# Performance work log

Hardware: AMD Instinct MI355X
Metric: run time of the kernel (lower is better)

Reference implementation:

```python
import jax, jax.numpy as jnp
import numpy as np

# Detect() defaults from the source
NUM_CLASSES = 2
TOP_K = 750          # max detections returned per class
NMS_TOP_K = 5000     # candidates considered by NMS
NMS_THRESH = 0.3
CONF_THRESH = 0.05
VAR0, VAR1 = 0.1, 0.2  # prior box variances


def decode(loc, priors):
    # loc, priors: [P,4]; priors in (cx,cy,w,h); returns corner boxes [P,4]
    xy = priors[:, :2] + loc[:, :2] * VAR0 * priors[:, 2:]
    wh = priors[:, 2:] * jnp.exp(loc[:, 2:] * VAR1)
    x1y1 = xy - wh * 0.5
    x2y2 = x1y1 + wh
    return jnp.concatenate([x1y1, x2y2], axis=1)


def nms_single(boxes, scores):
    # boxes [P,4], scores [P] -> kept rows [TOP_K,5] = (score, x1,y1,x2,y2)
    s = jnp.where(scores > CONF_THRESH, scores, -1.0)
    top_s, top_i = jax.lax.top_k(s, NMS_TOP_K)   # restrict to best nms_top_k candidates
    cb = boxes[top_i]                             # [K,4] candidate boxes
    area = (cb[:, 2] - cb[:, 0]) * (cb[:, 3] - cb[:, 1])
    ar = jnp.arange(NMS_TOP_K)

    def step(s_cur, _):
        i = jnp.argmax(s_cur)                     # highest-scoring unsuppressed box
        sc = s_cur[i]
        ok = sc > 0.0                             # any valid candidate left?
        b = cb[i]
        xx1 = jnp.maximum(cb[:, 0], b[0])
        yy1 = jnp.maximum(cb[:, 1], b[1])
        xx2 = jnp.minimum(cb[:, 2], b[2])
        yy2 = jnp.minimum(cb[:, 3], b[3])
        inter = jnp.clip(xx2 - xx1, 0.0) * jnp.clip(yy2 - yy1, 0.0)
        union = area - inter + area[i]
        iou = inter / union
        supp = (iou > NMS_THRESH) | (ar == i)     # suppress overlapping + self
        s_next = jnp.where(ok & supp, -1.0, s_cur)
        row = jnp.where(ok, jnp.concatenate([sc[None], b]), jnp.zeros(5, boxes.dtype))
        return s_next, row

    _, rows = jax.lax.scan(step, top_s, None, length=TOP_K)
    return rows  # [TOP_K, 5]


def setup_inputs() -> dict:
    key = jax.random.key(0)
    k1, k2, k3 = jax.random.split(key, 3)
    B, P = 8, 136500
    loc_data = jax.random.normal(k1, (B, P, 4), jnp.float32)
    conf_data = jax.random.normal(k2, (B, P, 2), jnp.float32)
    u = jax.random.uniform(k3, (P, 4), jnp.float32)
    # priors: cx,cy in (0,1); w,h small positive (normalized coords)
    prior_data = jnp.concatenate([u[:, :2], u[:, 2:] * 0.1 + 0.01], axis=1)
    return {"loc_data": loc_data, "conf_data": conf_data, "prior_data": prior_data}


def reference(loc_data, conf_data, prior_data):
    B = loc_data.shape[0]
    conf = jax.nn.softmax(conf_data, axis=-1)                    # [B,P,2]
    boxes = jax.vmap(lambda l: decode(l, prior_data))(loc_data)  # [B,P,4]
    rows = jax.vmap(nms_single)(boxes, conf[:, :, 1])            # [B,TOP_K,5]
    out = jnp.zeros((B, NUM_CLASSES, TOP_K, 5), loc_data.dtype)  # class 0 = background, all zeros
    out = out.at[:, 1].set(rows)
    return out
```

## Files before the change

kernel.cpp:

```cpp
#include <hip/hip_runtime.h>
#include <stdint.h>

#pragma clang fp contract(off)

#define NPRI   136500
#define BATCH  8
#define NMS_K  5000
#define NKPAD  5120
#define TOPK   750
#define SORT_N 8192
#define HBINS  1024
#define HOFF   0x3D40
#define MROW   80
#define CNTSTRIDE 32
#define CUT    32

typedef unsigned long long u64;

__device__ __forceinline__ u64 shfl64(u64 v, int src) {
    int lo = __shfl((int)(unsigned)(v & 0xffffffffull), src);
    int hi = __shfl((int)(unsigned)(v >> 32), src);
    return ((u64)(unsigned)hi << 32) | (u64)(unsigned)lo;
}
__device__ __forceinline__ u64 shfl64_xor(u64 v, int m) {
    int lo = __shfl_xor((int)(unsigned)(v & 0xffffffffull), m);
    int hi = __shfl_xor((int)(unsigned)(v >> 32), m);
    return ((u64)(unsigned)hi << 32) | (u64)(unsigned)lo;
}

__device__ __forceinline__ bool iou_sup(float4 c4, float aj,
                                        float4 rbx, float ra) {
    float xx1 = fmaxf(c4.x, rbx.x);
    float yy1 = fmaxf(c4.y, rbx.y);
    float xx2 = fminf(c4.z, rbx.z);
    float yy2 = fminf(c4.w, rbx.w);
    float iw = fmaxf(xx2 - xx1, 0.0f);
    float ih = fmaxf(yy2 - yy1, 0.0f);
    float inter = iw * ih;
    float uni = (aj - inter) + ra;
    float u = fmaf(-0.3f, uni, inter);
    float d = fmaf(-1.4901161193847656e-8f, uni, u);
    return d > 0.0f;
}
__device__ __forceinline__ u64 iou_word(float4 c4, float aj,
                                        float4 rbx, float ra) {
    return __ballot(iou_sup(c4, aj, rbx, ra));
}

__device__ __forceinline__ u64 diag_mask(u64 word, int sh) {
    if (sh >= 0)
        word &= (sh >= 63) ? 0ull : (~0ull << (sh + 1));
    return word;
}

__device__ u64 row_word_slow(const float4* __restrict__ cbp,
                             const float* __restrict__ cap,
                             float4 rbx, float ra, int W) {
    int jbase = W << 6;
    u64 word = 0ull;
    for (int jj = 0; jj < 64; ++jj) {
        int jc = min(jbase + jj, NMS_K - 1);
        if (iou_sup(cbp[jc], cap[jc], rbx, ra)) word |= (1ull << jj);
    }
    return word;
}

__global__ __launch_bounds__(256) void score_hist_kernel(
        const float* __restrict__ conf, unsigned int* __restrict__ hist,
        float* __restrict__ sraw) {
    int b = blockIdx.y;
    __shared__ unsigned int h[HBINS];
    for (int i = threadIdx.x; i < HBINS; i += 256) h[i] = 0;
    __syncthreads();
    for (int p = blockIdx.x * 256 + threadIdx.x; p < NPRI; p += 64 * 256) {
        float2 c = ((const float2*)conf)[(size_t)b * NPRI + p];
        float m  = fmaxf(c.x, c.y);
        float e0 = expf(c.x - m), e1 = expf(c.y - m);
        float s  = e1 / (e0 + e1);
        sraw[(size_t)b * NPRI + p] = s;
        if (s > 0.05f) {
            int bin = (int)(__float_as_uint(s) >> 16) - HOFF;
            bin = min(max(bin, 0), HBINS - 1);
            atomicAdd(&h[bin], 1u);
        }
    }
    __syncthreads();
    for (int i = threadIdx.x; i < HBINS; i += 256) {
        unsigned int v = h[i];
        if (v) atomicAdd(&hist[b * HBINS + i], v);
    }
}

__global__ __launch_bounds__(256) void compact_kernel(
        const float* __restrict__ sraw, const unsigned int* __restrict__ hist,
        u64* __restrict__ keys, unsigned int* __restrict__ cnt) {
    int b = blockIdx.y;
    int tid = threadIdx.x;
    int lane = tid & 63;
    __shared__ u64 buf[2304];
    __shared__ unsigned int hsum[256];
    __shared__ int best_sh;
    __shared__ unsigned int nloc;
    __shared__ unsigned int base_sh;
    const unsigned int* hb = hist + b * HBINS;
    int t4 = tid * 4;
    unsigned int h0 = hb[t4], h1 = hb[t4 + 1], h2 = hb[t4 + 2], h3 = hb[t4 + 3];
    hsum[tid] = h0 + h1 + h2 + h3;
    if (tid == 0) { best_sh = 0; nloc = 0; }
    __syncthreads();
    for (int o = 1; o < 256; o <<= 1) {
        unsigned int add = (tid + o < 256) ? hsum[tid + o] : 0u;
        __syncthreads();
        hsum[tid] += add;
        __syncthreads();
    }
    unsigned int nxt = (tid + 1 < 256) ? hsum[tid + 1] : 0u;
    unsigned int s3 = h3 + nxt;
    unsigned int s2 = h2 + s3;
    unsigned int s1 = h1 + s2;
    unsigned int s0 = h0 + s1;
    int cand = -1;
    if (s3 >= (unsigned)NMS_K) cand = t4 + 3;
    else if (s2 >= (unsigned)NMS_K) cand = t4 + 2;
    else if (s1 >= (unsigned)NMS_K) cand = t4 + 1;
    else if (s0 >= (unsigned)NMS_K) cand = t4;
    if (cand > 0) atomicMax(&best_sh, cand);
    __syncthreads();
    int tb = best_sh;
    for (int p = blockIdx.x * 256 + tid; p < NPRI; p += 64 * 256) {
        float s = sraw[(size_t)b * NPRI + p];
        bool pass = false;
        unsigned int bits = 0;
        if (s > 0.05f) {
            bits = __float_as_uint(s);
            int bin = (int)(bits >> 16) - HOFF;
            bin = min(max(bin, 0), HBINS - 1);
            pass = (bin >= tb);
        }
        u64 bal = __ballot(pass);
        int rank = (int)__popcll(bal & ((1ull << lane) - 1ull));
        unsigned int wbase = 0;
        if (lane == 0 && bal)
            wbase = atomicAdd(&nloc, (unsigned)__popcll(bal));
        wbase = (unsigned)__shfl((int)wbase, 0);
        if (pass)
            buf[wbase + rank] = ((u64)bits << 32) | (u64)(~(unsigned int)p);
    }
    __syncthreads();
    unsigned int tot = nloc;
    if (tid == 0)
        base_sh = tot ? atomicAdd(&cnt[b * CNTSTRIDE], tot) : 0u;
    __syncthreads();
    unsigned int base = base_sh;
    for (unsigned int i = tid; i < tot; i += 256) {
        unsigned int pos = base + i;
        if (pos < SORT_N)
            keys[(size_t)b * SORT_N + pos] = buf[i];
    }
}

__global__ __launch_bounds__(512) void sortmerge2k_kernel(
        const u64* __restrict__ keys, u64* __restrict__ keys2,
        const unsigned int* __restrict__ cnt) {
    int b = blockIdx.y, c = blockIdx.x;
    int tid = threadIdx.x;
    int lane = tid & 63;
    int wv = tid >> 6;
    int n = min((int)cnt[b * CNTSTRIDE], SORT_N);
    int base = c * 2048;
    if (base >= n) {
        for (int i = tid; i < 2048; i += 512)
            keys2[(size_t)b * SORT_N + base + i] = 0ull;
        return;
    }
    __shared__ u64 k[2048];
    __shared__ u64 k2[2048];
    for (int ch = wv; ch < 32; ch += 8) {
        int idx = base + ch * 64 + lane;
        u64 v = (idx < n) ? keys[(size_t)b * SORT_N + idx] : 0ull;
#pragma unroll
        for (int kk = 2; kk <= 64; kk <<= 1) {
#pragma unroll
            for (int j = kk >> 1; j > 0; j >>= 1) {
                u64 o = shfl64_xor(v, j);
                bool low  = (lane & j) == 0;
                bool desc = (lane & kk) == 0;
                u64 mx = (v >= o) ? v : o;
                u64 mn = (v >= o) ? o : v;
                v = desc ? (low ? mx : mn) : (low ? mn : mx);
            }
        }
        k[ch * 64 + lane] = v;
    }
    __syncthreads();
    u64* src = k;
    u64* dst = k2;
    for (int L = 64; L < 2048; L <<= 1) {
        for (int o = tid; o < 2048; o += 512) {
            int pair = o / (2 * L);
            int oo = o - pair * 2 * L;
            const u64* A  = src + pair * 2 * L;
            const u64* Bp = A + L;
            int lo = max(0, oo - L), hi = min(oo, L);
            while (lo < hi) {
                int mid = (lo + hi + 1) >> 1;
                bool ok = (oo - mid >= L) || (A[mid - 1] >= Bp[oo - mid]);
                if (ok) lo = mid; else hi = mid - 1;
            }
            int i = lo, j = oo - lo;
            u64 v;
            if (j >= L) v = A[i];
            else if (i >= L) v = Bp[j];
            else v = (A[i] >= Bp[j]) ? A[i] : Bp[j];
            dst[o] = v;
        }
        __syncthreads();
        u64* t = src; src = dst; dst = t;
    }
    for (int i = tid; i < 2048; i += 512)
        keys2[(size_t)b * SORT_N + base + i] = src[i];
}

__global__ __launch_bounds__(256) void merge1_kernel(
        const u64* __restrict__ keys2, u64* __restrict__ keys) {
    int b = blockIdx.y;
    int o = blockIdx.x * 256 + threadIdx.x;
    int pair = o >> 12;
    int oo = o & 4095;
    const u64* A  = keys2 + (size_t)b * SORT_N + pair * 4096;
    const u64* Bp = A + 2048;
    int lo = max(0, oo - 2048), hi = min(oo, 2048);
    while (lo < hi) {
        int mid = (lo + hi + 1) >> 1;
        bool ok = (oo - mid >= 2048) || (A[mid - 1] >= Bp[oo - mid]);
        if (ok) lo = mid; else hi = mid - 1;
    }
    int i = lo, j = oo - lo;
    u64 v;
    if (j >= 2048) v = A[i];
    else if (i >= 2048) v = Bp[j];
    else v = (A[i] >= Bp[j]) ? A[i] : Bp[j];
    keys[(size_t)b * SORT_N + pair * 4096 + oo] = v;
}

__global__ __launch_bounds__(256) void merge2_decode_kernel(
        const u64* __restrict__ keys,
        const float* __restrict__ loc, const float* __restrict__ priors,
        float* __restrict__ cscore, float* __restrict__ cbox,
        float* __restrict__ carea) {
    int b = blockIdx.y;
    int o = blockIdx.x * 256 + threadIdx.x;
    const u64* A  = keys + (size_t)b * SORT_N;
    const u64* Bp = A + 4096;
    int lo = max(0, o - 4096), hi = min(o, 4096);
    while (lo < hi) {
        int mid = (lo + hi + 1) >> 1;
        bool ok = (o - mid >= 4096) || (A[mid - 1] >= Bp[o - mid]);
        if (ok) lo = mid; else hi = mid - 1;
    }
    int i = lo, j = o - lo;
    u64 key;
    if (j >= 4096) key = A[i];
    else if (i >= 4096) key = Bp[j];
    else key = (A[i] >= Bp[j]) ? A[i] : Bp[j];
    if (o >= NMS_K) return;
    float sc; int idx;
    if (key != 0ull) {
        sc  = __uint_as_float((unsigned int)(key >> 32));
        idx = (int)(~(unsigned int)key);
    } else { sc = -1.0f; idx = 0; }
    cscore[b * NMS_K + o] = sc;
    float x1 = 0.f, y1 = 0.f, x2 = 0.f, y2 = 0.f, ar = 0.f;
    if (key != 0ull) {
        const float* l  = loc + ((size_t)b * NPRI + idx) * 4;
        const float* pr = priors + (size_t)idx * 4;
        float lx = l[0], ly = l[1], lw = l[2], lh = l[3];
        float pcx = pr[0], pcy = pr[1], pw = pr[2], ph = pr[3];
        float cx = pcx + (lx * 0.1f) * pw;
        float cy = pcy + (ly * 0.1f) * ph;
        float wd = pw * expf(lw * 0.2f);
        float ht = ph * expf(lh * 0.2f);
        x1 = cx - wd * 0.5f;  y1 = cy - ht * 0.5f;
        x2 = x1 + wd;         y2 = y1 + ht;
        ar = (x2 - x1) * (y2 - y1);
    }
    float* cb = cbox + ((size_t)b * NMS_K + o) * 4;
    cb[0] = x1; cb[1] = y1; cb[2] = x2; cb[3] = y2;
    carea[b * NMS_K + o] = ar;
}

__global__ __launch_bounds__(256, 4) void maskbuild_kernel(
        const float* __restrict__ cbox, const float* __restrict__ carea,
        u64* __restrict__ M) {
    int b   = blockIdx.y;
    int bid = blockIdx.x;
    int wgq, rb;
    if (bid >= 380) { wgq = 19; rb = bid - 380; }
    else {
        int w = (int)((sqrtf((float)(4 * bid + 5)) - 1.0f) * 0.5f);
        while (w * (w + 1) > bid) w--;
        while ((w + 1) * (w + 2) <= bid) w++;
        wgq = w; rb = bid - w * (w + 1);
    }
    int tid  = threadIdx.x;
    int lane = tid & 63;
    int wv   = __builtin_amdgcn_readfirstlane(tid >> 6);
    int w0   = wgq * 4;
    int rowbase = rb * 128;

    __shared__ float4 rbox[128];
    __shared__ float  rarea[128];
    if (tid < 128) {
        int i  = rowbase + tid;
        int ic = min(i, NMS_K - 1);
        rbox[tid]  = ((const float4*)cbox)[(size_t)b * NMS_K + ic];
        rarea[tid] = carea[(size_t)b * NMS_K + ic];
    }
    const float4* __restrict__ cbp = (const float4*)cbox + (size_t)b * NMS_K;
    const float*  __restrict__ cap = carea + (size_t)b * NMS_K;
    int j0 = w0 * 64 + lane;
    float4 c4_0 = cbp[min(j0,       NMS_K - 1)];
    float4 c4_1 = cbp[min(j0 +  64, NMS_K - 1)];
    float4 c4_2 = cbp[min(j0 + 128, NMS_K - 1)];
    float4 c4_3 = cbp[min(j0 + 192, NMS_K - 1)];
    float aj0 = cap[min(j0,       NMS_K - 1)];
    float aj1 = cap[min(j0 +  64, NMS_K - 1)];
    float aj2 = cap[min(j0 + 128, NMS_K - 1)];
    float aj3 = cap[min(j0 + 192, NMS_K - 1)];
    __syncthreads();

    int lr0 = 32 * wv;
    int rglob0 = rowbase + lr0;
    if (rglob0 >= NMS_K) return;

    u64* __restrict__ Mb = M + (size_t)b * NKPAD * MROW;

    if (rglob0 + 31 < w0 * 64) {
#pragma unroll 2
        for (int q = 0; q < 32; q += 2) {
            int lr = lr0 + q;
            float4 rb0 = rbox[lr], rb1 = rbox[lr + 1];
            float  ra0 = rarea[lr], ra1 = rarea[lr + 1];
            u64 A0 = iou_word(c4_0, aj0, rb0, ra0);
            u64 B0 = iou_word(c4_0, aj0, rb1, ra1);
            u64 A1 = iou_word(c4_1, aj1, rb0, ra0);
            u64 B1 = iou_word(c4_1, aj1, rb1, ra1);
            u64 A2 = iou_word(c4_2, aj2, rb0, ra0);
            u64 B2 = iou_word(c4_2, aj2, rb1, ra1);
            u64 A3 = iou_word(c4_3, aj3, rb0, ra0);
            u64 B3 = iou_word(c4_3, aj3, rb1, ra1);
            int row0 = rglob0 + q;
            if (lane == 0) {
                u64* d0 = Mb + (size_t)row0 * MROW + w0;
                ((ulonglong2*)d0)[0] = make_ulonglong2(A0, A1);
                ((ulonglong2*)d0)[1] = make_ulonglong2(A2, A3);
                u64* d1 = d0 + MROW;
                ((ulonglong2*)d1)[0] = make_ulonglong2(B0, B1);
                ((ulonglong2*)d1)[1] = make_ulonglong2(B2, B3);
            }
        }
    } else {
        int nrows = min(32, NMS_K - rglob0);
        int sh_base = rglob0 - w0 * 64;
#pragma unroll 2
        for (int q = 0; q < nrows; q += 2) {
            int lr = lr0 + q;
            float4 rb0 = rbox[lr], rb1 = rbox[lr + 1];
            float  ra0 = rarea[lr], ra1 = rarea[lr + 1];
            u64 A0 = iou_word(c4_0, aj0, rb0, ra0);
            u64 B0 = iou_word(c4_0, aj0, rb1, ra1);
            u64 A1 = iou_word(c4_1, aj1, rb0, ra0);
            u64 B1 = iou_word(c4_1, aj1, rb1, ra1);
            u64 A2 = iou_word(c4_2, aj2, rb0, ra0);
            u64 B2 = iou_word(c4_2, aj2, rb1, ra1);
            u64 A3 = iou_word(c4_3, aj3, rb0, ra0);
            u64 B3 = iou_word(c4_3, aj3, rb1, ra1);
            int sh = sh_base + q;
            A0 = diag_mask(A0, sh);       B0 = diag_mask(B0, sh + 1);
            A1 = diag_mask(A1, sh - 64);  B1 = diag_mask(B1, sh - 63);
            A2 = diag_mask(A2, sh - 128); B2 = diag_mask(B2, sh - 127);
            A3 = diag_mask(A3, sh - 192); B3 = diag_mask(B3, sh - 191);
            int row0 = rglob0 + q;
            if (lane == 0) {
                u64* d0 = Mb + (size_t)row0 * MROW + w0;
                ((ulonglong2*)d0)[0] = make_ulonglong2(A0, A1);
                ((ulonglong2*)d0)[1] = make_ulonglong2(A2, A3);
                u64* d1 = d0 + MROW;
                ((ulonglong2*)d1)[0] = make_ulonglong2(B0, B1);
                ((ulonglong2*)d1)[1] = make_ulonglong2(B2, B3);
            }
        }
    }
}

__global__ __launch_bounds__(1024) void maskscan_kernel(
        const float* __restrict__ cscore, const float* __restrict__ cbox,
        const float* __restrict__ carea,
        const unsigned int* __restrict__ cnt, const u64* __restrict__ M,
        float* __restrict__ out) {
    int b = blockIdx.x;
    int tid = threadIdx.x, lane = tid & 63, wv = tid >> 6;
    int nv = min((int)cnt[b * CNTSTRIDE], NMS_K);
    const u64* MB = M + (size_t)b * NKPAD * MROW;
    const float4* __restrict__ cbp = (const float4*)cbox + (size_t)b * NMS_K;
    const float*  __restrict__ cap = carea + (size_t)b * NMS_K;
    float* outb = out + (size_t)b * 2 * TOPK * 5;
    __shared__ unsigned int supp4[4];
    __shared__ u64 dbuf[2][64];
    __shared__ short allp[TOPK];
    __shared__ int emitted_sh;
    for (int i = tid; i < 2 * TOPK * 5; i += 1024) outb[i] = 0.f;
    if (tid < 4) supp4[tid] = 0u;
    if (tid == 0) emitted_sh = 0;
    if (wv == 1) dbuf[0][lane] = MB[(size_t)lane * MROW];
    __syncthreads();
    int emitted = 0;
    int nwords = (nv + 63) >> 6;
    u64 colw_prev = 0ull;
    u64 pickprev  = 0ull;
    for (int w = 0; w < nwords; w++) {
        int par = w & 1;
        if (wv == 0) {
            u64 colw;
            if (w + 1 < CUT) {
                colw = MB[(size_t)(w * 64 + lane) * MROW + (w + 1)];
            } else {
                int rc = min(w * 64 + lane, NMS_K - 1);
                colw = row_word_slow(cbp, cap, cbp[rc], cap[rc], w + 1);
            }
            u64 D = dbuf[par][lane];
            u64 sup = ((u64)supp4[2 * par + 1] << 32) | (u64)supp4[2 * par];
            if (lane == 0) {
                supp4[2 * par] = 0u;
                supp4[2 * par + 1] = 0u;
            }
            u64 x = ((pickprev >> lane) & 1ull) ? colw_prev : 0ull;
#pragma unroll
            for (int m = 1; m < 64; m <<= 1) x |= shfl64_xor(x, m);
            sup |= x;
            int base = w * 64, rem = nv - base;
            u64 valid = (rem >= 64) ? ~0ull : ((1ull << rem) - 1ull);
            u64 alive = valid & ~sup;
            u64 nz = __ballot(D != 0ull);
            u64 pickmask = 0ull;
            while (alive) {
                u64 blockers = alive & nz;
                if (!blockers) { pickmask |= alive; break; }
                int nb = __builtin_ctzll(blockers);
                u64 mle = (nb >= 63) ? ~0ull : ((1ull << (nb + 1)) - 1ull);
                pickmask |= alive & mle;
                u64 rw = shfl64(D, nb);
                alive &= ~mle;
                alive &= ~rw;
            }
            int room = TOPK - emitted;
            int pc = __popcll(pickmask);
            while (pc > room) {
                pickmask &= ~(1ull << (63 - __builtin_clzll(pickmask)));
                pc--;
            }
            if (lane == 0) emitted_sh = emitted + pc;
            if ((pickmask >> lane) & 1ull) {
                int rank = (int)__popcll(pickmask & ((1ull << lane) - 1ull));
                allp[emitted + rank] = (short)(base + lane);
            }
            pickprev = pickmask;
            colw_prev = colw;
        } else if (wv == 1) {
            if (w + 1 < nwords) {
                int W = w + 1;
                u64 dpre;
                if (W < CUT) {
                    dpre = MB[(size_t)(W * 64 + lane) * MROW + W];
                } else {
                    int rc = min(W * 64 + lane, NMS_K - 1);
                    dpre = diag_mask(
                        row_word_slow(cbp, cap, cbp[rc], cap[rc], W), lane);
                }
                dbuf[W & 1][lane] = dpre;
            }
        } else {
            int i = (wv - 2) * 64 + lane;
            u64 v = 0ull;
            if (i < emitted) {
                int pr = allp[i];
                if (w + 1 < CUT)
                    v = MB[(size_t)pr * MROW + (w + 1)];
                else
                    v = row_word_slow(cbp, cap, cbp[pr], cap[pr], w + 1);
            }
#pragma unroll
            for (int m = 1; m < 64; m <<= 1) v |= shfl64_xor(v, m);
            if (lane == 0 && v) {
                atomicOr(&supp4[2 * (par ^ 1)],     (unsigned int)v);
                atomicOr(&supp4[2 * (par ^ 1) + 1], (unsigned int)(v >> 32));
            }
        }
        __syncthreads();
        emitted = emitted_sh;
        if (emitted >= TOPK) break;
    }
    for (int t = tid; t < emitted; t += 1024) {
        int p = allp[t];
        float sc  = cscore[b * NMS_K + p];
        float4 bx = ((const float4*)cbox)[(size_t)b * NMS_K + p];
        float* o = outb + (size_t)(TOPK + t) * 5;
        o[0] = sc; o[1] = bx.x; o[2] = bx.y; o[3] = bx.z; o[4] = bx.w;
    }
}

extern "C" void kernel_launch(void* const* d_in, const int* in_sizes, int n_in,
                              void* d_out, int out_size, void* d_ws, size_t ws_size,
                              hipStream_t stream) {
    const float* loc    = (const float*)d_in[0];
    const float* conf   = (const float*)d_in[1];
    const float* priors = (const float*)d_in[2];
    float* out = (float*)d_out;

    char* ws = (char*)d_ws;
    size_t off = 0;
    unsigned int* hist = (unsigned int*)(ws + off);   off += (size_t)BATCH * HBINS * 4;
    unsigned int* cnt  = (unsigned int*)(ws + off);   off += (size_t)BATCH * CNTSTRIDE * 4;
    size_t zero_bytes = off;
    u64* keys  = (u64*)(ws + off);                    off += (size_t)BATCH * SORT_N * 8;
    u64* keys2 = (u64*)(ws + off);                    off += (size_t)BATCH * SORT_N * 8;
    float* cscore = (float*)(ws + off);               off += (size_t)BATCH * NMS_K * 4;
    float* cbox   = (float*)(ws + off);               off += (size_t)BATCH * NMS_K * 16;
    float* carea  = (float*)(ws + off);               off += (size_t)BATCH * NMS_K * 4;
    u64* M = (u64*)(ws + off);                        off += (size_t)BATCH * NKPAD * MROW * 8;
    float* sraw = (float*)M;

    hipMemsetAsync(d_ws, 0, zero_bytes, stream);

    score_hist_kernel<<<dim3(64, BATCH), 256, 0, stream>>>(conf, hist, sraw);
    compact_kernel<<<dim3(64, BATCH), 256, 0, stream>>>(sraw, hist, keys, cnt);
    sortmerge2k_kernel<<<dim3(4, BATCH), 512, 0, stream>>>(keys, keys2, cnt);
    merge1_kernel<<<dim3(32, BATCH), 256, 0, stream>>>(keys2, keys);
    merge2_decode_kernel<<<dim3(20, BATCH), 256, 0, stream>>>(keys, loc, priors, cscore, cbox, carea);
    maskbuild_kernel<<<dim3(72, BATCH), 256, 0, stream>>>(cbox, carea, M);
    maskscan_kernel<<<BATCH, 1024, 0, stream>>>(cscore, cbox, carea, cnt, M, out);
}
```

Before: 165.9 us.

## Sort 4K-element chunks in one block and drop separate merge1 kernel

The block-local sort grows from 2048 to 4096 keys per block with 1024 threads, which absorbs the 2048→4096 merge pass that merge1_kernel used to do, so one kernel launch and a global round trip go away. The merge-path binary search is also rewritten as a fixed-step, branch-free loop that interleaves four independent searches per thread to expose more memory-level parallelism in LDS. In exchange only 16 blocks run this stage (2 per batch), with 64KB of shared memory each, so it has less parallelism across the GPU and one extra merge level inside each block.

After: 175.6 us. 1.06x slower.

```diff
diff --git a/kernel.cpp b/kernel.cpp
--- a/kernel.cpp
+++ b/kernel.cpp
@@ -159,7 +159,7 @@
     }
 }
 
-__global__ __launch_bounds__(512) void sortmerge2k_kernel(
+__global__ __launch_bounds__(1024) void sortmerge4k_kernel(
         const u64* __restrict__ keys, u64* __restrict__ keys2,
         const unsigned int* __restrict__ cnt) {
     int b = blockIdx.y, c = blockIdx.x;
@@ -167,15 +167,15 @@
     int lane = tid & 63;
     int wv = tid >> 6;
     int n = min((int)cnt[b * CNTSTRIDE], SORT_N);
-    int base = c * 2048;
+    int base = c * 4096;
     if (base >= n) {
-        for (int i = tid; i < 2048; i += 512)
+        for (int i = tid; i < 4096; i += 1024)
             keys2[(size_t)b * SORT_N + base + i] = 0ull;
         return;
     }
-    __shared__ u64 k[2048];
-    __shared__ u64 k2[2048];
-    for (int ch = wv; ch < 32; ch += 8) {
+    __shared__ u64 k[4096];
+    __shared__ u64 k2[4096];
+    for (int ch = wv; ch < 64; ch += 16) {
         int idx = base + ch * 64 + lane;
         u64 v = (idx < n) ? keys[(size_t)b * SORT_N + idx] : 0ull;
 #pragma unroll
@@ -195,62 +195,59 @@
     __syncthreads();
     u64* src = k;
     u64* dst = k2;
-    for (int L = 64; L < 2048; L <<= 1) {
-        for (int o = tid; o < 2048; o += 512) {
+#pragma unroll 1
+    for (int L = 64; L < 4096; L <<= 1) {
+        int oo[4], lo[4], hi[4], Ao[4];
+#pragma unroll
+        for (int q = 0; q < 4; ++q) {
+            int o = tid + q * 1024;
             int pair = o / (2 * L);
-            int oo = o - pair * 2 * L;
-            const u64* A  = src + pair * 2 * L;
-            const u64* Bp = A + L;
-            int lo = max(0, oo - L), hi = min(oo, L);
-            while (lo < hi) {
-                int mid = (lo + hi + 1) >> 1;
-                bool ok = (oo - mid >= L) || (A[mid - 1] >= Bp[oo - mid]);
-                if (ok) lo = mid; else hi = mid - 1;
-            }
-            int i = lo, j = oo - lo;
+            Ao[q] = pair * 2 * L;
+            oo[q] = o - Ao[q];
+            lo[q] = max(0, oo[q] - L);
+            hi[q] = min(oo[q], L);
+        }
+        int nsteps = 32 - __builtin_clz(L);
+        for (int s = 0; s < nsteps; ++s) {
+#pragma unroll
+            for (int q = 0; q < 4; ++q) {
+                bool lv = lo[q] < hi[q];
+                int m = (lo[q] + hi[q] + 1) >> 1;
+                u64 a  = src[Ao[q] + max(m - 1, 0)];
+                u64 bb = src[Ao[q] + L + min(max(oo[q] - m, 0), L - 1)];
+                bool ok = (oo[q] - m >= L) || (a >= bb);
+                lo[q] = (lv && ok)  ? m     : lo[q];
+                hi[q] = (lv && !ok) ? m - 1 : hi[q];
+            }
+        }
+#pragma unroll
+        for (int q = 0; q < 4; ++q) {
+            int i = lo[q], j = oo[q] - lo[q];
             u64 v;
-            if (j >= L) v = A[i];
-            else if (i >= L) v = Bp[j];
-            else v = (A[i] >= Bp[j]) ? A[i] : Bp[j];
-            dst[o] = v;
+            if (j >= L) v = src[Ao[q] + i];
+            else if (i >= L) v = src[Ao[q] + L + j];
+            else {
+                u64 a = src[Ao[q] + i];
+                u64 bb = src[Ao[q] + L + j];
+                v = (a >= bb) ? a : bb;
+            }
+            dst[tid + q * 1024] = v;
         }
         __syncthreads();
         u64* t = src; src = dst; dst = t;
     }
-    for (int i = tid; i < 2048; i += 512)
+    for (int i = tid; i < 4096; i += 1024)
         keys2[(size_t)b * SORT_N + base + i] = src[i];
 }
 
-__global__ __launch_bounds__(256) void merge1_kernel(
-        const u64* __restrict__ keys2, u64* __restrict__ keys) {
-    int b = blockIdx.y;
-    int o = blockIdx.x * 256 + threadIdx.x;
-    int pair = o >> 12;
-    int oo = o & 4095;
-    const u64* A  = keys2 + (size_t)b * SORT_N + pair * 4096;
-    const u64* Bp = A + 2048;
-    int lo = max(0, oo - 2048), hi = min(oo, 2048);
-    while (lo < hi) {
-        int mid = (lo + hi + 1) >> 1;
-        bool ok = (oo - mid >= 2048) || (A[mid - 1] >= Bp[oo - mid]);
-        if (ok) lo = mid; else hi = mid - 1;
-    }
-    int i = lo, j = oo - lo;
-    u64 v;
-    if (j >= 2048) v = A[i];
-    else if (i >= 2048) v = Bp[j];
-    else v = (A[i] >= Bp[j]) ? A[i] : Bp[j];
-    keys[(size_t)b * SORT_N + pair * 4096 + oo] = v;
-}
-
 __global__ __launch_bounds__(256) void merge2_decode_kernel(
-        const u64* __restrict__ keys,
+        const u64* __restrict__ keys2,
         const float* __restrict__ loc, const float* __restrict__ priors,
         float* __restrict__ cscore, float* __restrict__ cbox,
         float* __restrict__ carea) {
     int b = blockIdx.y;
     int o = blockIdx.x * 256 + threadIdx.x;
-    const u64* A  = keys + (size_t)b * SORT_N;
+    const u64* A  = keys2 + (size_t)b * SORT_N;
     const u64* Bp = A + 4096;
     int lo = max(0, o - 4096), hi = min(o, 4096);
     while (lo < hi) {
@@ -534,9 +531,8 @@
 
     score_hist_kernel<<<dim3(64, BATCH), 256, 0, stream>>>(conf, hist, sraw);
     compact_kernel<<<dim3(64, BATCH), 256, 0, stream>>>(sraw, hist, keys, cnt);
-    sortmerge2k_kernel<<<dim3(4, BATCH), 512, 0, stream>>>(keys, keys2, cnt);
-    merge1_kernel<<<dim3(32, BATCH), 256, 0, stream>>>(keys2, keys);
-    merge2_decode_kernel<<<dim3(20, BATCH), 256, 0, stream>>>(keys, loc, priors, cscore, cbox, carea);
+    sortmerge4k_kernel<<<dim3(2, BATCH), 1024, 0, stream>>>(keys, keys2, cnt);
+    merge2_decode_kernel<<<dim3(20, BATCH), 256, 0, stream>>>(keys2, loc, priors, cscore, cbox, carea);
     maskbuild_kernel<<<dim3(72, BATCH), 256, 0, stream>>>(cbox, carea, M);
     maskscan_kernel<<<BATCH, 1024, 0, stream>>>(cscore, cbox, carea, cnt, M, out);
 }
```
